# Kernel tuning notes

Measured on AMD Instinct MI355X. Metric: run time of the kernel, lower is better.

The kernel has to match this reference:

```python
import jax, jax.numpy as jnp
import numpy as np

EMBED_DIM = 768
NUM_HEADS = 32
B = 4
N = 512


def setup_inputs() -> dict:
    key = jax.random.key(0)
    ks = jax.random.split(key, 11)
    s = 0.02  # param init scale
    E = EMBED_DIM
    return {
        "query": jax.random.normal(ks[0], (B, N, E), jnp.float32),
        "attn_bias": jax.random.normal(ks[1], (B * NUM_HEADS, N, N), jnp.float32),
        "delta_pos": jax.random.normal(ks[2], (B, N, N, 3), jnp.float32),
        "Wq": jax.random.normal(ks[3], (E, E), jnp.float32) * s,
        "bq": jnp.zeros((E,), jnp.float32),
        "Wk": jax.random.normal(ks[4], (E, E), jnp.float32) * s,
        "bk": jnp.zeros((E,), jnp.float32),
        "Wv": jax.random.normal(ks[5], (E, E), jnp.float32) * s,
        "bv": jnp.zeros((E,), jnp.float32),
        # force_proj{1,2,3} stacked: row c is the Linear(E,1) weight for axis c
        "Wf": jax.random.normal(ks[6], (3, E), jnp.float32) * s,
        "bf": jnp.zeros((3,), jnp.float32),
    }


def reference(query, attn_bias, delta_pos, Wq, bq, Wk, bk, Wv, bv, Wf, bf):
    b, n, e = query.shape
    h = NUM_HEADS
    d = e // h
    scaling = d ** (-0.5)
    # projections -> (b, h, n, d)
    q = (query @ Wq.T + bq).reshape(b, n, h, d).transpose(0, 2, 1, 3) * scaling
    k = (query @ Wk.T + bk).reshape(b, n, h, d).transpose(0, 2, 1, 3)
    v = (query @ Wv.T + bv).reshape(b, n, h, d).transpose(0, 2, 1, 3)
    # attention scores + bias; dropout is identity in eval mode (p=0.1, training=False)
    attn = jnp.einsum("bhnd,bhmd->bhnm", q, k) + attn_bias.reshape(b, h, n, n)
    probs = jax.nn.softmax(attn, axis=-1)  # (b,h,n,m)
    # rotate probs by delta_pos (c in {x,y,z}) and contract with v over m
    # x[b,n,c,h,d] = sum_m probs[b,h,n,m] * delta_pos[b,n,m,c] * v[b,h,m,d]
    x = jnp.einsum("bhnm,bnmc,bhmd->bnchd", probs, delta_pos, v).reshape(b, n, 3, e)
    # per-axis force projection: Linear(E,1) for each spatial axis
    force = jnp.einsum("bnce,ce->bnc", x, Wf) + bf
    return force.astype(jnp.float32)
```

## Files before the change

### kernel.cpp

```cpp
#include <hip/hip_runtime.h>
#include <hip/hip_bf16.h>
#include <cstdint>
#include <cstddef>

#define EMBED 768
#define NHEAD 32
#define HDIM 24
#define DPAD 32
#define BATCH 4
#define SEQ 512
#define WCOLS 1632
#define NPADCOL 1664

typedef __attribute__((ext_vector_type(8))) short short8;
typedef __attribute__((ext_vector_type(4))) float f32x4;

static __device__ __forceinline__ unsigned short f2b(float v) {
    __hip_bfloat16 h = __float2bfloat16(v);
    return *reinterpret_cast<unsigned short*>(&h);
}

__global__ __launch_bounds__(256) void prep_w_kernel(
    const float* __restrict__ Wq, const float* __restrict__ Wk,
    const float* __restrict__ Wv, const float* __restrict__ Wf,
    const float* __restrict__ bq, const float* __restrict__ bkv,
    const float* __restrict__ bv,
    unsigned short* __restrict__ WcT, float* __restrict__ bcat)
{
    const float sc = 0.20412414523193154f;
    int j = blockIdx.x;
    #pragma unroll
    for (int rep = 0; rep < 3; ++rep) {
        int e = rep * 256 + threadIdx.x;
        float v;
        if (j < 768) {
            v = Wq[(size_t)j * EMBED + e] * sc;
        } else if (j < 1536) {
            v = Wk[(size_t)(j - 768) * EMBED + e];
        } else if (j < WCOLS) {
            int jc = j - 1536, h = jc / 3, c = jc - h * 3;
            float s = 0.f;
            #pragma unroll
            for (int d = 0; d < HDIM; ++d)
                s = fmaf(Wv[(size_t)(h * HDIM + d) * EMBED + e],
                         Wf[c * EMBED + h * HDIM + d], s);
            v = s;
        } else {
            v = 0.f;
        }
        WcT[(size_t)j * EMBED + e] = f2b(v);
    }
    if (threadIdx.x == 0) {
        float v = 0.f;
        if (j < 768) v = bq[j] * sc;
        else if (j < 1536) v = bkv[j - 768];
        else if (j < WCOLS) {
            int jc = j - 1536, h = jc / 3, c = jc - h * 3;
            float s = 0.f;
            #pragma unroll
            for (int d = 0; d < HDIM; ++d)
                s = fmaf(bv[h * HDIM + d], Wf[c * EMBED + h * HDIM + d], s);
            v = s;
        }
        bcat[j] = v;
    }
}

__global__ __launch_bounds__(256) void dtr_kernel(
    const float* __restrict__ delta, float* __restrict__ dtr)
{
    size_t u = (size_t)blockIdx.x * 256 + threadIdx.x;
    int m = (int)(u & 511);
    int n = (int)((u >> 9) & 511);
    int b = (int)(u >> 18);
    float d0 = delta[u * 3 + 0];
    float d1 = delta[u * 3 + 1];
    float d2 = delta[u * 3 + 2];
    dtr[((size_t)(b * 3 + 0) * SEQ + n) * SEQ + m] = d0;
    dtr[((size_t)(b * 3 + 1) * SEQ + n) * SEQ + m] = d1;
    dtr[((size_t)(b * 3 + 2) * SEQ + n) * SEQ + m] = d2;
}

#define LSTR 40
__global__ __launch_bounds__(256) void gemm_kernel(
    const float* __restrict__ Aq, const unsigned short* __restrict__ WcT,
    const float* __restrict__ bcat,
    unsigned short* __restrict__ qp, unsigned short* __restrict__ kp,
    float* __restrict__ vwb)
{
    __shared__ short As[2][64 * LSTR];
    __shared__ short Bs[2][64 * LSTR];
    int t = threadIdx.x;
    int lane = t & 63, wv = t >> 6;
    int l15 = lane & 15, lg = lane >> 4;
    int m0 = blockIdx.x * 64, n0 = blockIdx.y * 64;
    int wm = (wv >> 1) * 32, wn = (wv & 1) * 32;

    f32x4 acc[2][2];
    #pragma unroll
    for (int i = 0; i < 2; ++i)
        #pragma unroll
        for (int j = 0; j < 2; ++j) acc[i][j] = (f32x4){0.f, 0.f, 0.f, 0.f};

    int sr = t >> 2;
    int sc8 = (t & 3) * 8;
    const float* Ag = Aq + (size_t)(m0 + sr) * EMBED + sc8;
    const unsigned short* Bg = WcT + (size_t)(n0 + sr) * EMBED + sc8;
    int lidx = sr * LSTR + sc8;

    short8 fa, fb;
    {
        float4 a0 = *(const float4*)(Ag);
        float4 a1 = *(const float4*)(Ag + 4);
        union { unsigned short u[8]; short8 v; } r;
        r.u[0] = f2b(a0.x); r.u[1] = f2b(a0.y); r.u[2] = f2b(a0.z); r.u[3] = f2b(a0.w);
        r.u[4] = f2b(a1.x); r.u[5] = f2b(a1.y); r.u[6] = f2b(a1.z); r.u[7] = f2b(a1.w);
        fa = r.v;
        fb = *(const short8*)(Bg);
    }
    *(short8*)&As[0][lidx] = fa;
    *(short8*)&Bs[0][lidx] = fb;
    __syncthreads();

    for (int kt = 0; kt < EMBED / 32; ++kt) {
        int cur = kt & 1;
        bool more = (kt + 1) < EMBED / 32;
        if (more) {
            float4 a0 = *(const float4*)(Ag + (kt + 1) * 32);
            float4 a1 = *(const float4*)(Ag + (kt + 1) * 32 + 4);
            fb = *(const short8*)(Bg + (size_t)(kt + 1) * 32);
            union { unsigned short u[8]; short8 v; } r;
            r.u[0] = f2b(a0.x); r.u[1] = f2b(a0.y); r.u[2] = f2b(a0.z); r.u[3] = f2b(a0.w);
            r.u[4] = f2b(a1.x); r.u[5] = f2b(a1.y); r.u[6] = f2b(a1.z); r.u[7] = f2b(a1.w);
            fa = r.v;
        }
        short8 af[2], bfr[2];
        #pragma unroll
        for (int i = 0; i < 2; ++i) {
            af[i]  = *(const short8*)&As[cur][(wm + i * 16 + l15) * LSTR + lg * 8];
            bfr[i] = *(const short8*)&Bs[cur][(wn + i * 16 + l15) * LSTR + lg * 8];
        }
        #pragma unroll
        for (int mt = 0; mt < 2; ++mt)
            #pragma unroll
            for (int nt = 0; nt < 2; ++nt)
                acc[mt][nt] = __builtin_amdgcn_mfma_f32_16x16x32_bf16(
                    af[mt], bfr[nt], acc[mt][nt], 0, 0, 0);
        if (more) {
            *(short8*)&As[cur ^ 1][lidx] = fa;
            *(short8*)&Bs[cur ^ 1][lidx] = fb;
            __syncthreads();
        }
    }

    #pragma unroll
    for (int mt = 0; mt < 2; ++mt) {
        #pragma unroll
        for (int nt = 0; nt < 2; ++nt) {
            #pragma unroll
            for (int r = 0; r < 4; ++r) {
                int gm = m0 + wm + mt * 16 + lg * 4 + r;
                int gn = n0 + wn + nt * 16 + l15;
                float v = acc[mt][nt][r] + bcat[gn];
                int b = gm >> 9, ns = gm & 511;
                if (gn < 768) {
                    int h = gn / 24, d = gn - h * 24;
                    qp[((size_t)(b * NHEAD + h) * SEQ + ns) * DPAD + d] = f2b(v);
                } else if (gn < 1536) {
                    int j2 = gn - 768, h = j2 / 24, d = j2 - h * 24;
                    kp[((size_t)(b * NHEAD + h) * SEQ + ns) * DPAD + d] = f2b(v);
                } else if (gn < WCOLS) {
                    int jc = gn - 1536, h = jc / 3, c = jc - h * 3;
                    vwb[((size_t)(b * NHEAD + h) * 3 + c) * SEQ + ns] = v;
                }
            }
        }
    }
}

__global__ __launch_bounds__(256) void init_out_kernel(
    const float* __restrict__ bf, float* __restrict__ out)
{
    int i = blockIdx.x * 256 + threadIdx.x;
    if (i < BATCH * SEQ * 3) out[i] = bf[i - (i / 3) * 3];
}

__global__ __launch_bounds__(512) void attn_kernel(
    const unsigned short* __restrict__ qp, const unsigned short* __restrict__ kp,
    const float* __restrict__ vwb, const float* __restrict__ bias,
    const float* __restrict__ dtr, float* __restrict__ out)
{
    __shared__ float wred[8][16][3];
    int t = threadIdx.x, lane = t & 63, w = t >> 6;
    int l15 = lane & 15, lg = lane >> 4;
    int nbase = blockIdx.x * 16;
    int b = blockIdx.y;
    int bh = b * NHEAD + blockIdx.z * 8 + w;

    short8 aq = *(const short8*)(qp + ((size_t)bh * SEQ + nbase + l15) * DPAD + lg * 8);

    const unsigned short* kbase = kp + (size_t)bh * SEQ * DPAD + lg * 8;
    const float* vw0   = vwb + (size_t)bh * 3 * SEQ + l15;
    const float* bbase = bias + ((size_t)bh * SEQ + nbase + lg * 4) * SEQ + l15;
    const float* dbase = dtr + (size_t)b * 3 * SEQ * SEQ
                             + (size_t)(nbase + lg * 4) * SEQ + l15;

    float den[4] = {0.f, 0.f, 0.f, 0.f};
    float facu[4][3];
    #pragma unroll
    for (int r = 0; r < 4; ++r) { facu[r][0] = 0.f; facu[r][1] = 0.f; facu[r][2] = 0.f; }

    #pragma unroll 2
    for (int mt = 0; mt < SEQ / 16; ++mt) {
        int moff = mt * 16;
        short8 bk = *(const short8*)(kbase + (size_t)(moff + l15) * DPAD);
        f32x4 z = {0.f, 0.f, 0.f, 0.f};
        f32x4 acc = __builtin_amdgcn_mfma_f32_16x16x32_bf16(aq, bk, z, 0, 0, 0);
        float v0 = vw0[moff];
        float v1 = vw0[SEQ + moff];
        float v2 = vw0[2 * SEQ + moff];
        #pragma unroll
        for (int r = 0; r < 4; ++r) {
            float e = __expf(acc[r] + bbase[(size_t)r * SEQ + moff]);
            den[r] += e;
            facu[r][0] = fmaf(e * v0, dbase[(size_t)r * SEQ + moff], facu[r][0]);
            facu[r][1] = fmaf(e * v1, dbase[(size_t)SEQ * SEQ + r * SEQ + moff], facu[r][1]);
            facu[r][2] = fmaf(e * v2, dbase[(size_t)2 * SEQ * SEQ + r * SEQ + moff], facu[r][2]);
        }
    }

    #pragma unroll
    for (int r = 0; r < 4; ++r) {
        #pragma unroll
        for (int o = 1; o <= 8; o <<= 1) {
            den[r]     += __shfl_xor(den[r], o);
            facu[r][0] += __shfl_xor(facu[r][0], o);
            facu[r][1] += __shfl_xor(facu[r][1], o);
            facu[r][2] += __shfl_xor(facu[r][2], o);
        }
        float rd = __builtin_amdgcn_rcpf(den[r]);
        facu[r][0] *= rd; facu[r][1] *= rd; facu[r][2] *= rd;
    }
    if (l15 == 0) {
        #pragma unroll
        for (int r = 0; r < 4; ++r) {
            wred[w][lg * 4 + r][0] = facu[r][0];
            wred[w][lg * 4 + r][1] = facu[r][1];
            wred[w][lg * 4 + r][2] = facu[r][2];
        }
    }
    __syncthreads();
    if (t < 48) {
        int n = t / 3, c = t - n * 3;
        float s = 0.f;
        #pragma unroll
        for (int ww = 0; ww < 8; ++ww) s += wred[ww][n][c];
        atomicAdd(&out[(size_t)(b * SEQ + nbase + n) * 3 + c], s);
    }
}

extern "C" void kernel_launch(void* const* d_in, const int* in_sizes, int n_in,
                              void* d_out, int out_size, void* d_ws, size_t ws_size,
                              hipStream_t stream)
{
    const float* query = (const float*)d_in[0];
    const float* attn_bias = (const float*)d_in[1];
    const float* delta = (const float*)d_in[2];
    const float* Wq = (const float*)d_in[3];
    const float* bq = (const float*)d_in[4];
    const float* Wk = (const float*)d_in[5];
    const float* bk = (const float*)d_in[6];
    const float* Wv = (const float*)d_in[7];
    const float* bv = (const float*)d_in[8];
    const float* Wf = (const float*)d_in[9];
    const float* bf = (const float*)d_in[10];
    float* out = (float*)d_out;

    uint8_t* p = (uint8_t*)d_ws;
    unsigned short* qp  = (unsigned short*)p; p += (size_t)BATCH * NHEAD * SEQ * DPAD * 2;
    unsigned short* kp  = (unsigned short*)p; p += (size_t)BATCH * NHEAD * SEQ * DPAD * 2;
    unsigned short* WcT = (unsigned short*)p; p += (size_t)NPADCOL * EMBED * 2;
    float* bcat = (float*)p;                  p += (size_t)NPADCOL * 4;
    float* vwb  = (float*)p;                  p += (size_t)BATCH * NHEAD * 3 * SEQ * 4;
    float* dtr  = (float*)p;                  p += (size_t)BATCH * 3 * SEQ * SEQ * 4;

    hipMemsetAsync(qp, 0, (size_t)BATCH * NHEAD * SEQ * DPAD * 2 * 2, stream);

    hipLaunchKernelGGL(prep_w_kernel, dim3(NPADCOL), dim3(256), 0, stream,
                       Wq, Wk, Wv, Wf, bq, bk, bv, WcT, bcat);
    hipLaunchKernelGGL(dtr_kernel, dim3((BATCH * SEQ * SEQ) / 256), dim3(256),
                       0, stream, delta, dtr);
    hipLaunchKernelGGL(gemm_kernel, dim3((BATCH * SEQ) / 64, NPADCOL / 64),
                       dim3(256), 0, stream, query, WcT, bcat, qp, kp, vwb);
    hipLaunchKernelGGL(init_out_kernel, dim3((BATCH * SEQ * 3 + 255) / 256),
                       dim3(256), 0, stream, bf, out);
    hipLaunchKernelGGL(attn_kernel, dim3(SEQ / 16, BATCH, 4), dim3(512), 0, stream,
                       qp, kp, vwb, attn_bias, dtr, out);
}
```

Baseline: 289.1 us.

## Split attention over key halves, pad delta to float4, pre-convert query to bf16

```diff
diff --git a/kernel.cpp b/kernel.cpp
--- a/kernel.cpp
+++ b/kernel.cpp
@@ -66,24 +66,34 @@
     }
 }
 
-__global__ __launch_bounds__(256) void dtr_kernel(
-    const float* __restrict__ delta, float* __restrict__ dtr)
-{
-    size_t u = (size_t)blockIdx.x * 256 + threadIdx.x;
-    int m = (int)(u & 511);
-    int n = (int)((u >> 9) & 511);
-    int b = (int)(u >> 18);
-    float d0 = delta[u * 3 + 0];
-    float d1 = delta[u * 3 + 1];
-    float d2 = delta[u * 3 + 2];
-    dtr[((size_t)(b * 3 + 0) * SEQ + n) * SEQ + m] = d0;
-    dtr[((size_t)(b * 3 + 1) * SEQ + n) * SEQ + m] = d1;
-    dtr[((size_t)(b * 3 + 2) * SEQ + n) * SEQ + m] = d2;
+__global__ __launch_bounds__(256) void qconv_kernel(
+    const float* __restrict__ q, unsigned short* __restrict__ o)
+{
+    size_t i = ((size_t)blockIdx.x * 256 + threadIdx.x) * 8;
+    float4 a = *(const float4*)(q + i);
+    float4 b = *(const float4*)(q + i + 4);
+    union { unsigned short u[8]; short8 v; } r;
+    r.u[0] = f2b(a.x); r.u[1] = f2b(a.y); r.u[2] = f2b(a.z); r.u[3] = f2b(a.w);
+    r.u[4] = f2b(b.x); r.u[5] = f2b(b.y); r.u[6] = f2b(b.z); r.u[7] = f2b(b.w);
+    *(short8*)(o + i) = r.v;
+}
+
+__global__ __launch_bounds__(256) void dtr4_kernel(
+    const float* __restrict__ delta, float* __restrict__ dtr4)
+{
+    __shared__ float st[768];
+    int t = threadIdx.x;
+    size_t u0 = (size_t)blockIdx.x * 256;
+    const float* src = delta + u0 * 3;
+    st[t] = src[t]; st[t + 256] = src[t + 256]; st[t + 512] = src[t + 512];
+    __syncthreads();
+    float4 o = { st[t * 3], st[t * 3 + 1], st[t * 3 + 2], 0.f };
+    *(float4*)(dtr4 + (u0 + t) * 4) = o;
 }
 
 #define LSTR 40
 __global__ __launch_bounds__(256) void gemm_kernel(
-    const float* __restrict__ Aq, const unsigned short* __restrict__ WcT,
+    const unsigned short* __restrict__ Aq, const unsigned short* __restrict__ WcT,
     const float* __restrict__ bcat,
     unsigned short* __restrict__ qp, unsigned short* __restrict__ kp,
     float* __restrict__ vwb)
@@ -104,20 +114,12 @@
 
     int sr = t >> 2;
     int sc8 = (t & 3) * 8;
-    const float* Ag = Aq + (size_t)(m0 + sr) * EMBED + sc8;
+    const unsigned short* Ag = Aq + (size_t)(m0 + sr) * EMBED + sc8;
     const unsigned short* Bg = WcT + (size_t)(n0 + sr) * EMBED + sc8;
     int lidx = sr * LSTR + sc8;
 
-    short8 fa, fb;
-    {
-        float4 a0 = *(const float4*)(Ag);
-        float4 a1 = *(const float4*)(Ag + 4);
-        union { unsigned short u[8]; short8 v; } r;
-        r.u[0] = f2b(a0.x); r.u[1] = f2b(a0.y); r.u[2] = f2b(a0.z); r.u[3] = f2b(a0.w);
-        r.u[4] = f2b(a1.x); r.u[5] = f2b(a1.y); r.u[6] = f2b(a1.z); r.u[7] = f2b(a1.w);
-        fa = r.v;
-        fb = *(const short8*)(Bg);
-    }
+    short8 fa = *(const short8*)(Ag);
+    short8 fb = *(const short8*)(Bg);
     *(short8*)&As[0][lidx] = fa;
     *(short8*)&Bs[0][lidx] = fb;
     __syncthreads();
@@ -126,13 +128,8 @@
         int cur = kt & 1;
         bool more = (kt + 1) < EMBED / 32;
         if (more) {
-            float4 a0 = *(const float4*)(Ag + (kt + 1) * 32);
-            float4 a1 = *(const float4*)(Ag + (kt + 1) * 32 + 4);
-            fb = *(const short8*)(Bg + (size_t)(kt + 1) * 32);
-            union { unsigned short u[8]; short8 v; } r;
-            r.u[0] = f2b(a0.x); r.u[1] = f2b(a0.y); r.u[2] = f2b(a0.z); r.u[3] = f2b(a0.w);
-            r.u[4] = f2b(a1.x); r.u[5] = f2b(a1.y); r.u[6] = f2b(a1.z); r.u[7] = f2b(a1.w);
-            fa = r.v;
+            fa = *(const short8*)(Ag + (kt + 1) * 32);
+            fb = *(const short8*)(Bg + (kt + 1) * 32);
         }
         short8 af[2], bfr[2];
         #pragma unroll
@@ -178,32 +175,25 @@
     }
 }
 
-__global__ __launch_bounds__(256) void init_out_kernel(
-    const float* __restrict__ bf, float* __restrict__ out)
-{
-    int i = blockIdx.x * 256 + threadIdx.x;
-    if (i < BATCH * SEQ * 3) out[i] = bf[i - (i / 3) * 3];
-}
-
 __global__ __launch_bounds__(512) void attn_kernel(
     const unsigned short* __restrict__ qp, const unsigned short* __restrict__ kp,
     const float* __restrict__ vwb, const float* __restrict__ bias,
-    const float* __restrict__ dtr, float* __restrict__ out)
-{
-    __shared__ float wred[8][16][3];
+    const float* __restrict__ dtr4, float* __restrict__ part)
+{
     int t = threadIdx.x, lane = t & 63, w = t >> 6;
     int l15 = lane & 15, lg = lane >> 4;
-    int nbase = blockIdx.x * 16;
+    int nbase = (blockIdx.x & 31) * 16;
+    int ms = blockIdx.x >> 5;
     int b = blockIdx.y;
     int bh = b * NHEAD + blockIdx.z * 8 + w;
+    int mbase = ms * 256;
 
     short8 aq = *(const short8*)(qp + ((size_t)bh * SEQ + nbase + l15) * DPAD + lg * 8);
 
-    const unsigned short* kbase = kp + (size_t)bh * SEQ * DPAD + lg * 8;
-    const float* vw0   = vwb + (size_t)bh * 3 * SEQ + l15;
-    const float* bbase = bias + ((size_t)bh * SEQ + nbase + lg * 4) * SEQ + l15;
-    const float* dbase = dtr + (size_t)b * 3 * SEQ * SEQ
-                             + (size_t)(nbase + lg * 4) * SEQ + l15;
+    const unsigned short* kbase = kp + ((size_t)bh * SEQ + mbase) * DPAD + lg * 8;
+    const float* vwp = vwb + (size_t)bh * 3 * SEQ + mbase + l15;
+    const float* bb  = bias + ((size_t)bh * SEQ + nbase + lg * 4) * SEQ + mbase + l15;
+    const float* db  = dtr4 + ((size_t)(b * SEQ + nbase + lg * 4) * SEQ + mbase + l15) * 4;
 
     float den[4] = {0.f, 0.f, 0.f, 0.f};
     float facu[4][3];
@@ -211,21 +201,22 @@
     for (int r = 0; r < 4; ++r) { facu[r][0] = 0.f; facu[r][1] = 0.f; facu[r][2] = 0.f; }
 
     #pragma unroll 2
-    for (int mt = 0; mt < SEQ / 16; ++mt) {
+    for (int mt = 0; mt < 16; ++mt) {
         int moff = mt * 16;
         short8 bk = *(const short8*)(kbase + (size_t)(moff + l15) * DPAD);
         f32x4 z = {0.f, 0.f, 0.f, 0.f};
         f32x4 acc = __builtin_amdgcn_mfma_f32_16x16x32_bf16(aq, bk, z, 0, 0, 0);
-        float v0 = vw0[moff];
-        float v1 = vw0[SEQ + moff];
-        float v2 = vw0[2 * SEQ + moff];
+        float v0 = vwp[moff];
+        float v1 = vwp[SEQ + moff];
+        float v2 = vwp[2 * SEQ + moff];
         #pragma unroll
         for (int r = 0; r < 4; ++r) {
-            float e = __expf(acc[r] + bbase[(size_t)r * SEQ + moff]);
+            float4 d = *(const float4*)(db + ((size_t)r * SEQ + moff) * 4);
+            float e = __expf(acc[r] + bb[(size_t)r * SEQ + moff]);
             den[r] += e;
-            facu[r][0] = fmaf(e * v0, dbase[(size_t)r * SEQ + moff], facu[r][0]);
-            facu[r][1] = fmaf(e * v1, dbase[(size_t)SEQ * SEQ + r * SEQ + moff], facu[r][1]);
-            facu[r][2] = fmaf(e * v2, dbase[(size_t)2 * SEQ * SEQ + r * SEQ + moff], facu[r][2]);
+            facu[r][0] = fmaf(e * v0, d.x, facu[r][0]);
+            facu[r][1] = fmaf(e * v1, d.y, facu[r][1]);
+            facu[r][2] = fmaf(e * v2, d.z, facu[r][2]);
         }
     }
 
@@ -238,25 +229,35 @@
             facu[r][1] += __shfl_xor(facu[r][1], o);
             facu[r][2] += __shfl_xor(facu[r][2], o);
         }
-        float rd = __builtin_amdgcn_rcpf(den[r]);
-        facu[r][0] *= rd; facu[r][1] *= rd; facu[r][2] *= rd;
     }
     if (l15 == 0) {
         #pragma unroll
         for (int r = 0; r < 4; ++r) {
-            wred[w][lg * 4 + r][0] = facu[r][0];
-            wred[w][lg * 4 + r][1] = facu[r][1];
-            wred[w][lg * 4 + r][2] = facu[r][2];
-        }
-    }
-    __syncthreads();
-    if (t < 48) {
-        int n = t / 3, c = t - n * 3;
-        float s = 0.f;
-        #pragma unroll
-        for (int ww = 0; ww < 8; ++ww) s += wred[ww][n][c];
-        atomicAdd(&out[(size_t)(b * SEQ + nbase + n) * 3 + c], s);
-    }
+            int n = nbase + lg * 4 + r;
+            float4 o = { facu[r][0], facu[r][1], facu[r][2], den[r] };
+            *(float4*)(part + (((size_t)bh * SEQ + n) * 2 + ms) * 4) = o;
+        }
+    }
+}
+
+__global__ __launch_bounds__(256) void combine_kernel(
+    const float* __restrict__ part, const float* __restrict__ bf,
+    float* __restrict__ out)
+{
+    int u = blockIdx.x * 256 + threadIdx.x;
+    if (u >= BATCH * SEQ * 3) return;
+    int c = u % 3;
+    int n = (u / 3) & 511;
+    int b = u / (SEQ * 3);
+    float s = 0.f;
+    #pragma unroll 4
+    for (int h = 0; h < NHEAD; ++h) {
+        const float* p = part + (((size_t)(b * NHEAD + h) * SEQ + n) * 2) * 4;
+        float f = p[c] + p[4 + c];
+        float d = p[3] + p[7];
+        s += f / d;
+    }
+    out[u] = s + bf[c];
 }
 
 extern "C" void kernel_launch(void* const* d_in, const int* in_sizes, int n_in,
@@ -277,23 +278,27 @@
     float* out = (float*)d_out;
 
     uint8_t* p = (uint8_t*)d_ws;
-    unsigned short* qp  = (unsigned short*)p; p += (size_t)BATCH * NHEAD * SEQ * DPAD * 2;
-    unsigned short* kp  = (unsigned short*)p; p += (size_t)BATCH * NHEAD * SEQ * DPAD * 2;
-    unsigned short* WcT = (unsigned short*)p; p += (size_t)NPADCOL * EMBED * 2;
-    float* bcat = (float*)p;                  p += (size_t)NPADCOL * 4;
-    float* vwb  = (float*)p;                  p += (size_t)BATCH * NHEAD * 3 * SEQ * 4;
-    float* dtr  = (float*)p;                  p += (size_t)BATCH * 3 * SEQ * SEQ * 4;
+    unsigned short* qp   = (unsigned short*)p; p += (size_t)BATCH * NHEAD * SEQ * DPAD * 2;
+    unsigned short* kp   = (unsigned short*)p; p += (size_t)BATCH * NHEAD * SEQ * DPAD * 2;
+    unsigned short* qb16 = (unsigned short*)p; p += (size_t)BATCH * SEQ * EMBED * 2;
+    unsigned short* WcT  = (unsigned short*)p; p += (size_t)NPADCOL * EMBED * 2;
+    float* bcat = (float*)p;                   p += (size_t)NPADCOL * 4;
+    float* vwb  = (float*)p;                   p += (size_t)BATCH * NHEAD * 3 * SEQ * 4;
+    float* dtr4 = (float*)p;                   p += (size_t)BATCH * SEQ * SEQ * 4 * 4;
+    float* part = (float*)p;                   p += (size_t)BATCH * NHEAD * SEQ * 2 * 4 * 4;
 
     hipMemsetAsync(qp, 0, (size_t)BATCH * NHEAD * SEQ * DPAD * 2 * 2, stream);
 
     hipLaunchKernelGGL(prep_w_kernel, dim3(NPADCOL), dim3(256), 0, stream,
                        Wq, Wk, Wv, Wf, bq, bk, bv, WcT, bcat);
-    hipLaunchKernelGGL(dtr_kernel, dim3((BATCH * SEQ * SEQ) / 256), dim3(256),
-                       0, stream, delta, dtr);
+    hipLaunchKernelGGL(qconv_kernel, dim3((BATCH * SEQ * EMBED) / (256 * 8)),
+                       dim3(256), 0, stream, query, qb16);
+    hipLaunchKernelGGL(dtr4_kernel, dim3((BATCH * SEQ * SEQ) / 256), dim3(256),
+                       0, stream, delta, dtr4);
     hipLaunchKernelGGL(gemm_kernel, dim3((BATCH * SEQ) / 64, NPADCOL / 64),
-                       dim3(256), 0, stream, query, WcT, bcat, qp, kp, vwb);
-    hipLaunchKernelGGL(init_out_kernel, dim3((BATCH * SEQ * 3 + 255) / 256),
-                       dim3(256), 0, stream, bf, out);
-    hipLaunchKernelGGL(attn_kernel, dim3(SEQ / 16, BATCH, 4), dim3(512), 0, stream,
-                       qp, kp, vwb, attn_bias, dtr, out);
-}
+                       dim3(256), 0, stream, qb16, WcT, bcat, qp, kp, vwb);
+    hipLaunchKernelGGL(attn_kernel, dim3(64, BATCH, 4), dim3(512), 0, stream,
+                       qp, kp, vwb, attn_bias, dtr4, part);
+    hipLaunchKernelGGL(combine_kernel, dim3((BATCH * SEQ * 3 + 255) / 256),
+                       dim3(256), 0, stream, part, bf, out);
+}
```

Measured after the change: 290.8 us. No clear change (+0.6%).
